# Optimization experiments

Hardware: AMD Instinct MI355X
Metric: run time of the kernel (lower is better)

The kernel has to match this reference:

```python
import jax, jax.numpy as jnp
import numpy as np

B, T, D = 1, 1024, 1024
H = 16; HKV = 16; HD = D // H; R = 2; K = 3; LOWR = 32
HR = HKV * R                      # heads after harmonic expansion
OUTW = HKV * HD * 2 * R           # w_proj output width
SCALE = HD ** -0.5


def setup_inputs() -> dict:
    key = jax.random.key(0)
    ks = jax.random.split(key, 10)
    def rn(k, shape, sc=1.0):
        return jax.random.normal(k, shape, dtype=jnp.float32) * sc
    return {
        'hidden_states': rn(ks[0], (B, T, D)),
        'q_w': rn(ks[1], (D, D), D ** -0.5),
        'k_w': rn(ks[2], (D, D), D ** -0.5),
        'v_w': rn(ks[3], (D, D), D ** -0.5),
        'w1': rn(ks[4], (LOWR, D), D ** -0.5),
        'w2': rn(ks[5], (OUTW, LOWR), LOWR ** -0.5),
        'conv_w': rn(ks[6], (OUTW, K), K ** -0.5),
        'bt_w': rn(ks[7], (HKV * R, D), D ** -0.5),
        'bt_b': jnp.zeros((HKV * R,), jnp.float32),
        'o_w': rn(ks[8], (D, D * R), (D * R) ** -0.5),
        'omega': 0.01 * jnp.ones((1, 1, 1, R), jnp.float32),
        'phi': jnp.zeros((1, 1, 1, R), jnp.float32),
    }


def path_attention_forward(hidden_states, q_w, k_w, v_w, w1, w2, conv_w,
                           bt_w, bt_b, o_w, omega, phi):
    b, t, _ = hidden_states.shape
    q = hidden_states @ q_w.T
    k = hidden_states @ k_w.T
    v = hidden_states @ v_w.T
    # low-rank w projection, causal depthwise short conv (kernel K), SiLU
    w_raw = (hidden_states @ w1.T) @ w2.T                    # [b,t,OUTW]
    xp = jnp.pad(w_raw, ((0, 0), (K - 1, 0), (0, 0)))
    w_raw = sum(xp[:, i:i + t, :] * conv_w[:, i] for i in range(K))
    w_raw = jax.nn.silu(w_raw)
    # rotary-like harmonic mixing of Householder directions
    w5 = w_raw.reshape(b, t, HKV, 2 * R, HD)
    Ah = w5[:, :, :, 0::2, :]                                # [b,t,HKV,R,HD]
    Bh = w5[:, :, :, 1::2, :]
    pos = jnp.arange(t, dtype=jnp.float32)[None, :, None, None]
    theta = omega * pos + phi                                # [1,t,1,R]
    c = jnp.cos(theta)[..., None]
    s = jnp.sin(theta)[..., None]
    Wdir = Ah * c + Bh * s
    Wdir = Wdir * jax.lax.rsqrt(jnp.sum(Wdir * Wdir, -1, keepdims=True) + 1e-6)
    beta = jax.nn.sigmoid(hidden_states @ bt_w.T + bt_b) * 2.0   # [b,t,HR]
    # repeat-interleave q/k/v heads across harmonics -> [b,HR,t,HD]
    to_h = lambda x: jnp.swapaxes(jnp.repeat(x.reshape(b, t, H, HD), R, axis=2), 1, 2)
    qh, kh, vh = to_h(q), to_h(k), to_h(v)
    wh = jnp.swapaxes(Wdir.reshape(b, t, HR, HD), 1, 2)      # [b,HR,t,HD]
    bh = jnp.swapaxes(beta, 1, 2)                            # [b,HR,t]
    # PaTH logits: A_ij = q_i^T (H_i ... H_{j+1}) k_j, H_t = I - beta_t w_t w_t^T.
    # WY/UT transform: with M_ts = beta_t (w_t.w_s) for s<t, the coefficients
    # B_tj (t>j) of the accumulated rank-1 corrections solve the unit-lower
    # triangular system (I + M) B = strilow(Db W K^T), and
    # A = tril(Q K^T - tril(Q W^T) B).
    idx = jnp.arange(t)
    strict = idx[:, None] > idx[None, :]
    incl = idx[:, None] >= idx[None, :]
    Mw = jnp.where(strict, jnp.einsum('bhtd,bhsd->bhts', wh, wh) * bh[..., None], 0.0)
    rhs = jnp.where(strict, jnp.einsum('bhtd,bhjd->bhtj', wh, kh) * bh[..., None], 0.0)
    Bmat = jax.scipy.linalg.solve_triangular(Mw + jnp.eye(t, dtype=Mw.dtype), rhs, lower=True)
    qk = jnp.einsum('bhid,bhjd->bhij', qh, kh)
    qw = jnp.where(incl, jnp.einsum('bhid,bhtd->bhit', qh, wh), 0.0)
    logits = (qk - jnp.einsum('bhit,bhtj->bhij', qw, Bmat)) * SCALE
    logits = jnp.where(incl, logits, -1e30)
    p = jax.nn.softmax(logits, axis=-1)
    o = jnp.einsum('bhij,bhjd->bhid', p, vh)                 # [b,HR,t,HD]
    o = jnp.swapaxes(o, 1, 2).reshape(b, t, HR * HD)         # [b,t,D*R]
    return o @ o_w.T


def reference(hidden_states, q_w, k_w, v_w, w1, w2, conv_w, bt_w, bt_b, o_w, omega, phi):
    return path_attention_forward(hidden_states, q_w, k_w, v_w, w1, w2, conv_w,
                                  bt_w, bt_b, o_w, omega, phi)
```

## Files before the change

kernel.cpp:

```cpp
#include <hip/hip_runtime.h>
#include <math.h>

#define TTD 1024
#define DDM 1024
#define HDIM 64
#define NOUTW 4096
#define PSCALE 0.125f
#define PSC2 0.18033688011112042f
#define LS 72

typedef __attribute__((ext_vector_type(8))) __bf16 bf16x8;
typedef __attribute__((ext_vector_type(4))) float f32x4;
#define MFMA16(a,b,c) __builtin_amdgcn_mfma_f32_16x16x32_bf16(a,b,c,0,0,0)

#define STR_(x) #x
#define WAITVM(N) asm volatile("s_waitcnt vmcnt(" STR_(N) ")" ::: "memory")
#define BAR() do { __builtin_amdgcn_s_barrier(); asm volatile("" ::: "memory"); } while (0)
#define LGKBAR() do { asm volatile("s_waitcnt lgkmcnt(0)" ::: "memory"); \
                      __builtin_amdgcn_s_barrier(); asm volatile("" ::: "memory"); } while (0)
#define FULLBAR() do { asm volatile("s_waitcnt vmcnt(0) lgkmcnt(0)" ::: "memory"); \
                       __builtin_amdgcn_s_barrier(); asm volatile("" ::: "memory"); } while (0)

__device__ __forceinline__ ushort f2b(float f) {
  unsigned u = __builtin_bit_cast(unsigned, f);
  return (ushort)((u + 0x7fffu + ((u >> 16) & 1u)) >> 16);
}
__device__ __forceinline__ float b2f(ushort u) {
  unsigned v = (unsigned)u << 16;
  return __builtin_bit_cast(float, v);
}

__device__ __forceinline__ void gload_lds16(const ushort* g, ushort* l) {
  __builtin_amdgcn_global_load_lds(
      (const __attribute__((address_space(1))) unsigned*)g,
      (__attribute__((address_space(3))) unsigned*)l, 16, 0, 0);
}

#define SWZ(row, cc) (((row) * 8 + ((cc) ^ ((row) & 7))) * 8)
#define SWZE(row, col) (SWZ(row, (col) >> 3) + ((col) & 7))

__device__ __forceinline__ void stage_tile(const ushort* gb, long gs, ushort* tile,
                                           int w, int l) {
  int sub = l >> 3, cc = (l & 7) ^ sub;
  #pragma unroll
  for (int it = 0; it < 2; ++it) {
    int q = w * 2 + it;
    gload_lds16(gb + (long)(q * 8 + sub) * gs + cc * 8, &tile[(q * 64 + l) * 8]);
  }
}

__device__ __forceinline__ bf16x8 frag(const ushort* tile, int row, int cc) {
  return *(const bf16x8*)&tile[SWZ(row, cc)];
}

#define OFF_X     0L
#define OFF_PZ    67108864L
#define OFF_HSB   67108864L
#define OFF_QWW   69206016L
#define OFF_KWW   71303168L
#define OFF_VWW   73400320L
#define OFF_W2B   75497472L
#define OFF_WLOWB 75759616L
#define OFF_TB    130023424L
#define OFF_OALL  130023424L
#define OFF_YB    134217728L
#define OFF_OWB   134217728L
#define OFF_WHB   138412032L
#define OFF_QB    142606336L
#define OFF_KB    144703488L
#define OFF_VTB   146800640L
#define OFF_BETA  148897792L
#define OFF_BW64  149159936L

__global__ __launch_bounds__(256) void cvt_kernel(const float* __restrict__ x,
                                                  ushort* __restrict__ y, long n) {
  long i = ((long)blockIdx.x * 256 + threadIdx.x) * 4;
  if (i >= n) return;
  float4 f = *(const float4*)(x + i);
  ushort4 o;
  o.x = f2b(f.x); o.y = f2b(f.y); o.z = f2b(f.z); o.w = f2b(f.w);
  *(ushort4*)(y + i) = o;
}

#define CVT_TOTAL 4390912L
struct CvtSegs {
  const float* src[7];
  ushort* dst[7];
  long cnt[7];
};
__global__ __launch_bounds__(256) void cvt_all_kernel(CvtSegs sg) {
  long e = ((long)blockIdx.x * 256 + threadIdx.x) * 4;
  #pragma unroll
  for (int s = 0; s < 7; ++s) {
    if (e < sg.cnt[s]) {
      float4 f = *(const float4*)(sg.src[s] + e);
      ushort4 o;
      o.x = f2b(f.x); o.y = f2b(f.y); o.z = f2b(f.z); o.w = f2b(f.w);
      *(ushort4*)(sg.dst[s] + e) = o;
      return;
    }
    e -= sg.cnt[s];
  }
}

__global__ __launch_bounds__(256) void qkv_sp_kernel(
    const ushort* __restrict__ hsb,
    const ushort* __restrict__ wq, const ushort* __restrict__ wk, const ushort* __restrict__ wv,
    const ushort* __restrict__ bw, const float* __restrict__ bt_b,
    ushort* __restrict__ cq, ushort* __restrict__ ck, ushort* __restrict__ cv,
    float* __restrict__ beta, ushort* __restrict__ wlowb)
{
  int z = blockIdx.z;
  if (z == 3 && blockIdx.x != 0) return;
  const ushort* B = (z == 0) ? wq : (z == 1) ? wk : (z == 2) ? wv : bw;

  __shared__ ushort Ab[2][8192];
  __shared__ ushort Bb[2][4096];

  int tid = threadIdx.x, w = tid >> 6, l = tid & 63;
  int quad = l >> 4, lane15 = l & 15;
  int rm = blockIdx.y * 128, cn = (z == 3) ? 0 : blockIdx.x * 64;
  const ushort* Ag = hsb + (long)rm * DDM;
  const ushort* Bg = B + (long)cn * DDM;

  stage_tile(Ag, DDM, &Ab[0][0], w, l);
  stage_tile(Ag + 64 * DDM, DDM, &Ab[0][4096], w, l);
  stage_tile(Bg, DDM, &Bb[0][0], w, l);

  f32x4 acc[2][4] = {};
  int arow0 = (w & 1) * 32 + lane15;
  int asel = (w >> 1) * 4096;
  for (int kt = 0; kt < 16; ++kt) {
    int cur = kt & 1;
    if (kt < 15) {
      int nxt = cur ^ 1;
      stage_tile(Ag + (kt + 1) * 64, DDM, &Ab[nxt][0], w, l);
      stage_tile(Ag + 64 * DDM + (kt + 1) * 64, DDM, &Ab[nxt][4096], w, l);
      stage_tile(Bg + (kt + 1) * 64, DDM, &Bb[nxt][0], w, l);
      WAITVM(6);
    } else {
      WAITVM(0);
    }
    BAR();
    const ushort* Atile = &Ab[cur][asel];
    #pragma unroll
    for (int s = 0; s < 2; ++s) {
      bf16x8 a0 = frag(Atile, arow0, s * 4 + quad);
      bf16x8 a1 = frag(Atile, arow0 + 16, s * 4 + quad);
      #pragma unroll
      for (int f = 0; f < 4; ++f) {
        bf16x8 bf = frag(&Bb[cur][0], f * 16 + lane15, s * 4 + quad);
        acc[0][f] = MFMA16(a0, bf, acc[0][f]);
        acc[1][f] = MFMA16(a1, bf, acc[1][f]);
      }
    }
    BAR();
  }

  if (z < 2) {
    ushort* Cb = (z == 0) ? cq : ck;
    #pragma unroll
    for (int rr = 0; rr < 2; ++rr) {
      int orow = rm + w * 32 + rr * 16 + quad * 4;
      #pragma unroll
      for (int f = 0; f < 4; ++f)
        #pragma unroll
        for (int r = 0; r < 4; ++r)
          Cb[(long)(orow + r) * DDM + cn + f * 16 + lane15] = f2b(acc[rr][f][r]);
    }
  } else if (z == 2) {
    #pragma unroll
    for (int rr = 0; rr < 2; ++rr) {
      int orow = rm + w * 32 + rr * 16 + quad * 4;
      #pragma unroll
      for (int f = 0; f < 4; ++f) {
        ushort4 o;
        o.x = f2b(acc[rr][f][0]); o.y = f2b(acc[rr][f][1]);
        o.z = f2b(acc[rr][f][2]); o.w = f2b(acc[rr][f][3]);
        *(ushort4*)&cv[(long)(cn + f * 16 + lane15) * TTD + orow] = o;
      }
    }
  } else {
    #pragma unroll
    for (int rr = 0; rr < 2; ++rr) {
      int orow = rm + w * 32 + rr * 16 + quad * 4;
      #pragma unroll
      for (int f = 0; f < 2; ++f) {
        int hr = f * 16 + lane15;
        float bb = bt_b[hr];
        #pragma unroll
        for (int r = 0; r < 4; ++r)
          beta[(long)hr * TTD + orow + r] = 2.f / (1.f + expf(-(acc[rr][f][r] + bb)));
      }
      #pragma unroll
      for (int f = 2; f < 4; ++f)
        #pragma unroll
        for (int r = 0; r < 4; ++r)
          wlowb[(long)(orow + r) * 32 + (f - 2) * 16 + lane15] = f2b(acc[rr][f][r]);
    }
  }
}

__global__ __launch_bounds__(256) void wrawconv_kernel(
    const ushort* __restrict__ wlowb, const ushort* __restrict__ w2b,
    const float* __restrict__ conv_w, const float* __restrict__ omega,
    const float* __restrict__ phi, ushort* __restrict__ whb)
{
  int rm = blockIdx.x * 64;
  int p = blockIdx.y;
  int hkv = p >> 1, r = p & 1;
  int c0 = hkv * 256 + r * 128;

  __shared__ ushort As[64 * 32];
  __shared__ ushort Bs[128 * 32];
  __shared__ float WR[66][132];

  int tid = threadIdx.x, w = tid >> 6, l = tid & 63;
  int quad = l >> 4, lane15 = l & 15;

  {
    int row = tid >> 2, ch = (tid & 3) * 8;
    gload_lds16(wlowb + (long)(rm + row) * 32 + ch, &As[row * 32 + ch]);
    gload_lds16(w2b + (long)(c0 + row) * 32 + ch, &Bs[row * 32 + ch]);
    gload_lds16(w2b + (long)(c0 + 64 + row) * 32 + ch, &Bs[(64 + row) * 32 + ch]);
  }
  {
    int hr2 = tid >> 7, col = tid & 127;
    float acc = 0.f;
    if (rm > 0) {
      long t = rm - 2 + hr2;
      for (int k = 0; k < 32; ++k)
        acc += b2f(wlowb[t * 32 + k]) * b2f(w2b[(long)(c0 + col) * 32 + k]);
    }
    WR[hr2][col] = acc;
  }
  FULLBAR();

  #pragma unroll
  for (int g = 0; g < 2; ++g) {
    f32x4 acc[4] = {};
    bf16x8 af = *(const bf16x8*)&As[(w * 16 + lane15) * 32 + quad * 8];
    #pragma unroll
    for (int f = 0; f < 4; ++f) {
      bf16x8 bf = *(const bf16x8*)&Bs[(g * 64 + f * 16 + lane15) * 32 + quad * 8];
      acc[f] = MFMA16(af, bf, acc[f]);
    }
    #pragma unroll
    for (int f = 0; f < 4; ++f)
      #pragma unroll
      for (int rr = 0; rr < 4; ++rr)
        WR[2 + w * 16 + quad * 4 + rr][g * 64 + f * 16 + lane15] = acc[f][rr];
  }
  LGKBAR();

  float cwa[3], cwb[3];
  #pragma unroll
  for (int i = 0; i < 3; ++i) {
    cwa[i] = conv_w[(long)(c0 + l) * 3 + i];
    cwb[i] = conv_w[(long)(c0 + 64 + l) * 3 + i];
  }
  float om = omega[r], ph = phi[r];
  for (int it = 0; it < 16; ++it) {
    int tl = it * 4 + w;
    int t = rm + tl;
    float a = cwa[0] * WR[tl][l] + cwa[1] * WR[tl + 1][l] + cwa[2] * WR[tl + 2][l];
    float b = cwb[0] * WR[tl][64 + l] + cwb[1] * WR[tl + 1][64 + l] + cwb[2] * WR[tl + 2][64 + l];
    a = a / (1.f + expf(-a));
    b = b / (1.f + expf(-b));
    float th = om * (float)t + ph;
    float wd = a * cosf(th) + b * sinf(th);
    float ss = wd * wd;
    #pragma unroll
    for (int o = 32; o > 0; o >>= 1) ss += __shfl_xor(ss, o, 64);
    whb[((long)p * TTD + t) * HDIM + l] = f2b(wd * (1.f / sqrtf(ss + 1e-6f)));
  }
}

__global__ __launch_bounds__(256) void solveA_kernel(
    const ushort* __restrict__ whb, const float* __restrict__ beta,
    ushort* __restrict__ TB, ushort* __restrict__ YB)
{
  int c = blockIdx.x, h = blockIdx.y;
  const ushort* whc = whb + ((long)h * TTD + c * 64) * HDIM;
  const float* bet = beta + (long)h * TTD + c * 64;
  ushort* TBh = TB + ((long)h * 16 + c) * 4096;
  ushort* YBh = YB + ((long)h * 16 + c) * 4096;

  __shared__ float Lm[64][65];
  __shared__ float Vf[64][65];
  __shared__ ushort WT[64 * LS];
  __shared__ ushort Tb[64 * LS];

  int tid = threadIdx.x, w = tid >> 6, l = tid & 63;
  int quad = l >> 4, lane15 = l & 15;

  f32x4 g[4] = {};
  #pragma unroll
  for (int s = 0; s < 2; ++s) {
    bf16x8 af = *(const bf16x8*)&whc[(long)(w * 16 + lane15) * HDIM + s * 32 + quad * 8];
    #pragma unroll
    for (int f = 0; f < 4; ++f) {
      bf16x8 bf = *(const bf16x8*)&whc[(long)(f * 16 + lane15) * HDIM + s * 32 + quad * 8];
      g[f] = MFMA16(af, bf, g[f]);
    }
  }
  #pragma unroll
  for (int r = 0; r < 4; ++r) {
    int t = w * 16 + quad * 4 + r;
    float bv = bet[t];
    #pragma unroll
    for (int f = 0; f < 4; ++f) {
      int tp = f * 16 + lane15;
      Lm[t][tp] = (t > tp) ? bv * g[f][r] : 0.f;
    }
  }
  {
    int d0 = (tid & 7) * 8;
    #pragma unroll
    for (int it = 0; it < 2; ++it) {
      int t = it * 32 + (tid >> 3);
      uint4 pk = *(const uint4*)&whc[(long)t * HDIM + d0];
      const ushort* pu = (const ushort*)&pk;
      #pragma unroll
      for (int i = 0; i < 8; ++i) WT[(d0 + i) * LS + t] = pu[i];
    }
  }
  LGKBAR();

  {
    float cur[16];
    #pragma unroll
    for (int i = 0; i < 16; ++i) cur[i] = (w * 16 + i == l) ? bet[l] : 0.f;
    for (int sb = 0; sb < 4; ++sb) {
      if (w == sb) {
        float xloc[16];
        #pragma unroll
        for (int i = 0; i < 16; ++i) {
          float bv = cur[i];
          #pragma unroll
          for (int j2 = 0; j2 < 16; ++j2)
            if (j2 < i) bv -= Lm[sb * 16 + i][sb * 16 + j2] * xloc[j2];
          xloc[i] = bv;
          Vf[sb * 16 + i][l] = bv;
        }
      }
      LGKBAR();
      if (w > sb) {
        float xp[16];
        #pragma unroll
        for (int t = 0; t < 16; ++t) xp[t] = Vf[sb * 16 + t][l];
        #pragma unroll
        for (int i = 0; i < 16; ++i) {
          float s2 = cur[i];
          #pragma unroll
          for (int t = 0; t < 16; ++t) s2 -= Lm[w * 16 + i][sb * 16 + t] * xp[t];
          cur[i] = s2;
        }
      }
    }
  }
  {
    int t = tid >> 2, off = (tid & 3) * 16;
    ushort tmp[16];
    #pragma unroll
    for (int i = 0; i < 16; ++i) { tmp[i] = f2b(Vf[t][off + i]); Tb[t * LS + off + i] = tmp[i]; }
    *(uint4*)&TBh[t * 64 + off] = *(const uint4*)&tmp[0];
    *(uint4*)&TBh[t * 64 + off + 8] = *(const uint4*)&tmp[8];
  }
  LGKBAR();
  f32x4 y[4] = {};
  #pragma unroll
  for (int s = 0; s < 2; ++s) {
    bf16x8 af = *(const bf16x8*)&Tb[(w * 16 + lane15) * LS + s * 32 + quad * 8];
    #pragma unroll
    for (int f = 0; f < 4; ++f) {
      bf16x8 bf = *(const bf16x8*)&WT[(f * 16 + lane15) * LS + s * 32 + quad * 8];
      y[f] = MFMA16(af, bf, y[f]);
    }
  }
  #pragma unroll
  for (int f = 0; f < 4; ++f)
    #pragma unroll
    for (int r = 0; r < 4; ++r)
      YBh[(long)(w * 16 + quad * 4 + r) * 64 + f * 16 + lane15] = f2b(y[f][r]);
}

__global__ __launch_bounds__(256) void solveB_kernel(
    const ushort* __restrict__ whb, const ushort* __restrict__ kb,
    const ushort* __restrict__ TB, const ushort* __restrict__ YB,
    ushort* __restrict__ Xb, ushort* __restrict__ KZ)
{
  int h = blockIdx.x;
  int ty = blockIdx.y;
  int js = (ty < 8) ? ty : (23 - ty);
  int j0 = js * 64;
  const ushort* wh_h = whb + (long)h * TTD * HDIM;
  const ushort* k_h = kb + (long)(h >> 1) * 64;
  ushort* X_h = Xb + (long)h * TTD * TTD;
  ushort* KZ_h = KZ + (long)h * 15 * TTD * HDIM;

  __shared__ ushort KT[4096];
  __shared__ ushort WT[4096];
  __shared__ ushort XM[4096];
  __shared__ ushort nS[4096];

  int tid = threadIdx.x, w = tid >> 6, l = tid & 63;
  int quad = l >> 4, lane15 = l & 15;
  f32x4 Sacc[4] = {}, Wacc[4] = {};

  stage_tile(k_h + (long)j0 * DDM, DDM, KT, w, l);

  float kreg[4][4];
  #pragma unroll
  for (int f = 0; f < 4; ++f)
    #pragma unroll
    for (int r = 0; r < 4; ++r)
      kreg[f][r] = b2f(k_h[(long)(j0 + w * 16 + quad * 4 + r) * DDM + f * 16 + lane15]);

  WAITVM(0);

  for (int c = js; c < 16; ++c) {
    const ushort* whc = wh_h + (long)c * 64 * HDIM;
    LGKBAR();
    {
      int d0 = (tid & 7) * 8;
      #pragma unroll
      for (int it = 0; it < 2; ++it) {
        int t = it * 32 + (tid >> 3);
        uint4 pk = *(const uint4*)&whc[(long)t * HDIM + d0];
        const ushort* pu = (const ushort*)&pk;
        #pragma unroll
        for (int i = 0; i < 8; ++i) WT[SWZE(d0 + i, t)] = pu[i];
      }
    }
    f32x4 xacc[4] = {};
    if (c == js) {
      f32x4 m[4] = {};
      #pragma unroll
      for (int s = 0; s < 2; ++s) {
        bf16x8 af = *(const bf16x8*)&whc[(long)(w * 16 + lane15) * HDIM + s * 32 + quad * 8];
        #pragma unroll
        for (int f = 0; f < 4; ++f)
          m[f] = MFMA16(af, frag(KT, f * 16 + lane15, s * 4 + quad), m[f]);
      }
      #pragma unroll
      for (int f = 0; f < 4; ++f)
        #pragma unroll
        for (int r = 0; r < 4; ++r) {
          int t = w * 16 + quad * 4 + r, j = f * 16 + lane15;
          XM[SWZE(j, t)] = (t > j) ? f2b(m[f][r]) : (ushort)0;
        }
      LGKBAR();
      const ushort* TBh = TB + ((long)h * 16 + c) * 4096;
      #pragma unroll
      for (int s = 0; s < 2; ++s) {
        bf16x8 af = *(const bf16x8*)&TBh[(long)(w * 16 + lane15) * 64 + s * 32 + quad * 8];
        #pragma unroll
        for (int f = 0; f < 4; ++f)
          xacc[f] = MFMA16(af, frag(XM, f * 16 + lane15, s * 4 + quad), xacc[f]);
      }
      LGKBAR();
    } else {
      const ushort* YBh = YB + ((long)h * 16 + c) * 4096;
      #pragma unroll
      for (int s = 0; s < 2; ++s) {
        bf16x8 af = *(const bf16x8*)&YBh[(long)(w * 16 + lane15) * 64 + s * 32 + quad * 8];
        #pragma unroll
        for (int f = 0; f < 4; ++f) {
          xacc[f] = MFMA16(af, frag(KT, f * 16 + lane15, s * 4 + quad), xacc[f]);
          xacc[f] = MFMA16(af, frag(nS, f * 16 + lane15, s * 4 + quad), xacc[f]);
        }
      }
    }
    #pragma unroll
    for (int f = 0; f < 4; ++f)
      #pragma unroll
      for (int r = 0; r < 4; ++r)
        XM[SWZE(f * 16 + lane15, w * 16 + quad * 4 + r)] = f2b(xacc[f][r]);
    LGKBAR();
    {
      int j = tid >> 2, c2 = (tid & 3) * 2;
      bf16x8 s0 = frag(XM, j, c2);
      bf16x8 s1 = frag(XM, j, c2 + 1);
      *(bf16x8*)&X_h[(long)(j0 + j) * TTD + c * 64 + c2 * 8] = s0;
      *(bf16x8*)&X_h[(long)(j0 + j) * TTD + c * 64 + c2 * 8 + 8] = s1;
    }
    if (c < 15) {
      #pragma unroll
      for (int s = 0; s < 2; ++s) {
        bf16x8 aw = frag(WT, w * 16 + lane15, s * 4 + quad);
        bf16x8 ax = frag(XM, w * 16 + lane15, s * 4 + quad);
        #pragma unroll
        for (int f = 0; f < 4; ++f) {
          Sacc[f] = MFMA16(aw, frag(XM, f * 16 + lane15, s * 4 + quad), Sacc[f]);
          Wacc[f] = MFMA16(ax, frag(WT, f * 16 + lane15, s * 4 + quad), Wacc[f]);
        }
      }
      ushort* pz = KZ_h + (long)c * TTD * HDIM;
      #pragma unroll
      for (int f = 0; f < 4; ++f)
        #pragma unroll
        for (int r = 0; r < 4; ++r)
          pz[(long)(j0 + w * 16 + quad * 4 + r) * 64 + f * 16 + lane15] =
              f2b(kreg[f][r] - Wacc[f][r]);
      #pragma unroll
      for (int f = 0; f < 4; ++f)
        #pragma unroll
        for (int r = 0; r < 4; ++r)
          nS[SWZE(f * 16 + lane15, w * 16 + quad * 4 + r)] = f2b(-Sacc[f][r]);
    }
  }
}

__global__ __launch_bounds__(256) void flash_kernel(
    const ushort* __restrict__ qb, const ushort* __restrict__ kbuf,
    const ushort* __restrict__ whb, const ushort* __restrict__ Xb,
    const ushort* __restrict__ KZ, const ushort* __restrict__ vTb,
    ushort* __restrict__ oall)
{
  int h = blockIdx.x;
  int y = blockIdx.y;
  int ri = (y < 8) ? y : (23 - y);
  int r0 = ri * 64;
  const ushort* q_h = qb + (long)(h >> 1) * 64;
  const ushort* k_h = kbuf + (long)(h >> 1) * 64;
  const ushort* wh_h = whb + (long)h * TTD * HDIM;
  const ushort* X_h = Xb + (long)h * TTD * TTD;
  const ushort* kz = KZ + ((long)h * 15 + (ri - 1)) * TTD * HDIM;
  const ushort* v_h = vTb + (long)(h >> 1) * 64 * TTD;

  __shared__ ushort S[2][3][4096];
  __shared__ ushort KD[4096];
  __shared__ ushort QWD[4096];
  __shared__ ushort PT[4096];

  int tid = threadIdx.x, w = tid >> 6, l = tid & 63;
  int quad = l >> 4, lane15 = l & 15;

  bf16x8 aq[2];
  #pragma unroll
  for (int s = 0; s < 2; ++s)
    aq[s] = *(const bf16x8*)&q_h[(long)(r0 + w * 16 + lane15) * DDM + s * 32 + quad * 8];
  stage_tile(k_h + (long)r0 * DDM, DDM, KD, w, l);
  if (ri > 0) stage_tile(kz, 64, &S[0][0][0], w, l);
  stage_tile(X_h + r0, TTD, &S[0][1][0], w, l);
  stage_tile(v_h, TTD, &S[0][2][0], w, l);
  {
    f32x4 t4[4] = {};
    #pragma unroll
    for (int s = 0; s < 2; ++s)
      #pragma unroll
      for (int f = 0; f < 4; ++f) {
        bf16x8 bf = *(const bf16x8*)&wh_h[(long)(r0 + f * 16 + lane15) * HDIM + s * 32 + quad * 8];
        t4[f] = MFMA16(aq[s], bf, t4[f]);
      }
    #pragma unroll
    for (int f = 0; f < 4; ++f)
      #pragma unroll
      for (int r = 0; r < 4; ++r) {
        int i = w * 16 + quad * 4 + r, t = f * 16 + lane15;
        QWD[SWZE(i, t)] = (i >= t) ? f2b(-t4[f][r]) : (ushort)0;
      }
  }

  f32x4 O[4] = {};
  float m[4], lsum[4];
  #pragma unroll
  for (int r = 0; r < 4; ++r) { m[r] = -1e30f; lsum[r] = 0.f; }

  for (int jb = 0; jb <= ri; ++jb) {
    int cur = jb & 1;
    if (jb < ri) {
      long c0n = (long)(jb + 1) * 64;
      ushort* nb = &S[cur ^ 1][0][0];
      if (jb + 1 < ri) {
        stage_tile(kz + c0n * 64, 64, nb, w, l);
        stage_tile(X_h + c0n * TTD + r0, TTD, nb + 4096, w, l);
        stage_tile(v_h + c0n, TTD, nb + 8192, w, l);
        WAITVM(6);
      } else {
        stage_tile(X_h + c0n * TTD + r0, TTD, nb + 4096, w, l);
        stage_tile(v_h + c0n, TTD, nb + 8192, w, l);
        WAITVM(4);
      }
    } else {
      WAITVM(0);
    }
    BAR();
    const ushort* Skz = &S[cur][0][0];
    const ushort* Sx  = &S[cur][1][0];
    const ushort* Sv  = &S[cur][2][0];
    f32x4 acc[4] = {};
    const ushort* Sb = (jb < ri) ? Skz : KD;
    #pragma unroll
    for (int s = 0; s < 2; ++s)
      #pragma unroll
      for (int f = 0; f < 4; ++f)
        acc[f] = MFMA16(aq[s], frag(Sb, f * 16 + lane15, s * 4 + quad), acc[f]);
    #pragma unroll
    for (int s = 0; s < 2; ++s) {
      bf16x8 aw = frag(QWD, w * 16 + lane15, s * 4 + quad);
      #pragma unroll
      for (int f = 0; f < 4; ++f)
        acc[f] = MFMA16(aw, frag(Sx, f * 16 + lane15, s * 4 + quad), acc[f]);
    }
    float rmax[4] = {-3e38f, -3e38f, -3e38f, -3e38f};
    #pragma unroll
    for (int f = 0; f < 4; ++f)
      #pragma unroll
      for (int r = 0; r < 4; ++r) {
        float lv = acc[f][r] * PSC2;
        if (jb == ri && (f * 16 + lane15) > (w * 16 + quad * 4 + r)) lv = -3e38f;
        acc[f][r] = lv;
        rmax[r] = fmaxf(rmax[r], lv);
      }
    #pragma unroll
    for (int r = 0; r < 4; ++r) {
      rmax[r] = fmaxf(rmax[r], __shfl_xor(rmax[r], 1, 64));
      rmax[r] = fmaxf(rmax[r], __shfl_xor(rmax[r], 2, 64));
      rmax[r] = fmaxf(rmax[r], __shfl_xor(rmax[r], 4, 64));
      rmax[r] = fmaxf(rmax[r], __shfl_xor(rmax[r], 8, 64));
    }
    float alpha[4], rs[4] = {0.f, 0.f, 0.f, 0.f};
    #pragma unroll
    for (int r = 0; r < 4; ++r) {
      float nm = fmaxf(m[r], rmax[r]);
      alpha[r] = exp2f(m[r] - nm);
      m[r] = nm;
    }
    #pragma unroll
    for (int f = 0; f < 4; ++f)
      #pragma unroll
      for (int r = 0; r < 4; ++r) {
        float e = exp2f(acc[f][r] - m[r]);
        acc[f][r] = e;
        rs[r] += e;
      }
    #pragma unroll
    for (int r = 0; r < 4; ++r) {
      rs[r] += __shfl_xor(rs[r], 1, 64);
      rs[r] += __shfl_xor(rs[r], 2, 64);
      rs[r] += __shfl_xor(rs[r], 4, 64);
      rs[r] += __shfl_xor(rs[r], 8, 64);
      lsum[r] = lsum[r] * alpha[r] + rs[r];
    }
    #pragma unroll
    for (int f = 0; f < 4; ++f)
      #pragma unroll
      for (int r = 0; r < 4; ++r) O[f][r] *= alpha[r];
    #pragma unroll
    for (int f = 0; f < 4; ++f)
      #pragma unroll
      for (int r = 0; r < 4; ++r) {
        int i = w * 16 + quad * 4 + r;
        PT[SWZE(i, f * 16 + lane15)] = f2b(acc[f][r]);
      }
    #pragma unroll
    for (int s = 0; s < 2; ++s) {
      bf16x8 ap = frag(PT, w * 16 + lane15, s * 4 + quad);
      #pragma unroll
      for (int f = 0; f < 4; ++f)
        O[f] = MFMA16(ap, frag(Sv, f * 16 + lane15, s * 4 + quad), O[f]);
    }
    BAR();
  }
  #pragma unroll
  for (int r = 0; r < 4; ++r) lsum[r] = 1.f / lsum[r];
  #pragma unroll
  for (int f = 0; f < 4; ++f)
    #pragma unroll
    for (int r = 0; r < 4; ++r)
      oall[(long)(r0 + w * 16 + quad * 4 + r) * 2048 + h * 64 + f * 16 + lane15] =
          f2b(O[f][r] * lsum[r]);
}

__global__ __launch_bounds__(256) void gemm_out_kernel(
    const ushort* __restrict__ A, const ushort* __restrict__ Bb, float* __restrict__ C)
{
  __shared__ ushort Ab[2][8192];
  __shared__ ushort Bt[2][8192];
  int tid = threadIdx.x, w = tid >> 6, l = tid & 63;
  int quad = l >> 4, lane15 = l & 15;
  int rm = blockIdx.y * 64, cn = blockIdx.x * 64;
  const ushort* Ag = A + (long)rm * 2048;
  const ushort* Bg = Bb + (long)cn * 2048;

  stage_tile(Ag, 2048, &Ab[0][0], w, l);
  stage_tile(Ag + 64, 2048, &Ab[0][4096], w, l);
  stage_tile(Bg, 2048, &Bt[0][0], w, l);
  stage_tile(Bg + 64, 2048, &Bt[0][4096], w, l);

  f32x4 acc[4] = {};
  for (int kt = 0; kt < 16; ++kt) {
    int cur = kt & 1;
    if (kt < 15) {
      int nxt = cur ^ 1;
      long o = (long)(kt + 1) * 128;
      stage_tile(Ag + o, 2048, &Ab[nxt][0], w, l);
      stage_tile(Ag + o + 64, 2048, &Ab[nxt][4096], w, l);
      stage_tile(Bg + o, 2048, &Bt[nxt][0], w, l);
      stage_tile(Bg + o + 64, 2048, &Bt[nxt][4096], w, l);
      WAITVM(8);
    } else {
      WAITVM(0);
    }
    BAR();
    #pragma unroll
    for (int u = 0; u < 2; ++u)
      #pragma unroll
      for (int s = 0; s < 2; ++s) {
        bf16x8 af = frag(&Ab[cur][u * 4096], w * 16 + lane15, s * 4 + quad);
        #pragma unroll
        for (int f = 0; f < 4; ++f)
          acc[f] = MFMA16(af, frag(&Bt[cur][u * 4096], f * 16 + lane15, s * 4 + quad), acc[f]);
      }
    BAR();
  }
  int orow = rm + w * 16 + quad * 4;
  #pragma unroll
  for (int f = 0; f < 4; ++f)
    #pragma unroll
    for (int r = 0; r < 4; ++r)
      C[(long)(orow + r) * DDM + cn + f * 16 + lane15] = acc[f][r];
}

extern "C" void kernel_launch(void* const* d_in, const int* in_sizes, int n_in,
                              void* d_out, int out_size, void* d_ws, size_t ws_size,
                              hipStream_t stream) {
  const float* hs     = (const float*)d_in[0];
  const float* q_w    = (const float*)d_in[1];
  const float* k_w    = (const float*)d_in[2];
  const float* v_w    = (const float*)d_in[3];
  const float* w1     = (const float*)d_in[4];
  const float* w2     = (const float*)d_in[5];
  const float* conv_w = (const float*)d_in[6];
  const float* bt_w   = (const float*)d_in[7];
  const float* bt_b   = (const float*)d_in[8];
  const float* o_w    = (const float*)d_in[9];
  const float* omega  = (const float*)d_in[10];
  const float* phi    = (const float*)d_in[11];
  float* out = (float*)d_out;
  char* ws = (char*)d_ws;

  ushort* Xb     = (ushort*)(ws + OFF_X);
  ushort* KZb    = (ushort*)(ws + OFF_PZ);
  ushort* hs_b   = (ushort*)(ws + OFF_HSB);
  ushort* qw_wb  = (ushort*)(ws + OFF_QWW);
  ushort* kw_wb  = (ushort*)(ws + OFF_KWW);
  ushort* vw_wb  = (ushort*)(ws + OFF_VWW);
  ushort* w2_b   = (ushort*)(ws + OFF_W2B);
  ushort* wlow_b = (ushort*)(ws + OFF_WLOWB);
  ushort* TB     = (ushort*)(ws + OFF_TB);
  ushort* o_all  = (ushort*)(ws + OFF_OALL);
  ushort* YB     = (ushort*)(ws + OFF_YB);
  ushort* ow_b   = (ushort*)(ws + OFF_OWB);
  ushort* wh_b   = (ushort*)(ws + OFF_WHB);
  ushort* q_b    = (ushort*)(ws + OFF_QB);
  ushort* k_b    = (ushort*)(ws + OFF_KB);
  ushort* vT_b   = (ushort*)(ws + OFF_VTB);
  float*  beta   = (float*)(ws + OFF_BETA);
  ushort* bw_b   = (ushort*)(ws + OFF_BW64);

  CvtSegs sg;
  sg.src[0] = hs;   sg.dst[0] = hs_b;          sg.cnt[0] = 1048576;
  sg.src[1] = q_w;  sg.dst[1] = qw_wb;         sg.cnt[1] = 1048576;
  sg.src[2] = k_w;  sg.dst[2] = kw_wb;         sg.cnt[2] = 1048576;
  sg.src[3] = v_w;  sg.dst[3] = vw_wb;         sg.cnt[3] = 1048576;
  sg.src[4] = w2;   sg.dst[4] = w2_b;          sg.cnt[4] = 131072;
  sg.src[5] = bt_w; sg.dst[5] = bw_b;          sg.cnt[5] = 32768;
  sg.src[6] = w1;   sg.dst[6] = bw_b + 32768;  sg.cnt[6] = 32768;
  cvt_all_kernel<<<dim3((CVT_TOTAL + 1023) / 1024), 256, 0, stream>>>(sg);

  qkv_sp_kernel<<<dim3(16, 8, 4), 256, 0, stream>>>(
      hs_b, qw_wb, kw_wb, vw_wb, bw_b, bt_b, q_b, k_b, vT_b, beta, wlow_b);

  wrawconv_kernel<<<dim3(16, 32), 256, 0, stream>>>(
      wlow_b, w2_b, conv_w, omega, phi, wh_b);

  solveA_kernel<<<dim3(16, 32), 256, 0, stream>>>(wh_b, beta, TB, YB);
  solveB_kernel<<<dim3(32, 16), 256, 0, stream>>>(wh_b, k_b, TB, YB, Xb, KZb);

  cvt_kernel<<<dim3(2048), 256, 0, stream>>>(o_w, ow_b, 2097152L);

  flash_kernel<<<dim3(32, 16), 256, 0, stream>>>(q_b, k_b, wh_b, Xb, KZb, vT_b, o_all);

  gemm_out_kernel<<<dim3(16, 16), 256, 0, stream>>>(o_all, ow_b, out);

  (void)in_sizes; (void)n_in; (void)out_size; (void)ws_size;
}
```

Baseline: 231.6 us.

## Fuse w-direction conv into solveA, pack X triangularly, merge o_w conversion

Merges the w-projection/conv/SiLU/normalise kernel with the chunk-local triangular solve, so the normalised directions stay in shared memory instead of being read back from global memory. It also stores the X matrix as packed lower-triangular 64x64 tiles per head rather than a dense T x T matrix, which shrinks the workspace and makes the flash kernel's tile loads contiguous. The separate o_w conversion launch is folded into the batched conversion kernel. In exchange, shared memory is reused through a hand-laid-out pool with aliased regions, which may lower occupancy and is fragile.

```diff
diff --git a/kernel.cpp b/kernel.cpp
--- a/kernel.cpp
+++ b/kernel.cpp
@@ -4,7 +4,6 @@
 #define TTD 1024
 #define DDM 1024
 #define HDIM 64
-#define NOUTW 4096
 #define PSCALE 0.125f
 #define PSC2 0.18033688011112042f
 #define LS 72
@@ -53,45 +52,36 @@
   return *(const bf16x8*)&tile[SWZ(row, cc)];
 }
 
+#define XT_PERH   557056L
 #define OFF_X     0L
-#define OFF_PZ    67108864L
-#define OFF_HSB   67108864L
-#define OFF_QWW   69206016L
-#define OFF_KWW   71303168L
-#define OFF_VWW   73400320L
-#define OFF_W2B   75497472L
-#define OFF_WLOWB 75759616L
-#define OFF_TB    130023424L
-#define OFF_OALL  130023424L
-#define OFF_YB    134217728L
-#define OFF_OWB   134217728L
-#define OFF_WHB   138412032L
-#define OFF_QB    142606336L
-#define OFF_KB    144703488L
-#define OFF_VTB   146800640L
-#define OFF_BETA  148897792L
-#define OFF_BW64  149159936L
-
-__global__ __launch_bounds__(256) void cvt_kernel(const float* __restrict__ x,
-                                                  ushort* __restrict__ y, long n) {
-  long i = ((long)blockIdx.x * 256 + threadIdx.x) * 4;
-  if (i >= n) return;
-  float4 f = *(const float4*)(x + i);
-  ushort4 o;
-  o.x = f2b(f.x); o.y = f2b(f.y); o.z = f2b(f.z); o.w = f2b(f.w);
-  *(ushort4*)(y + i) = o;
-}
-
-#define CVT_TOTAL 4390912L
+#define OFF_PZ    35651584L
+#define OFF_HSB   35651584L
+#define OFF_QWW   37748736L
+#define OFF_KWW   39845888L
+#define OFF_VWW   41943040L
+#define OFF_W2B   44040192L
+#define OFF_WLOWB 44302336L
+#define OFF_TB    98566144L
+#define OFF_OALL  98566144L
+#define OFF_YB    102760448L
+#define OFF_OWB   106954752L
+#define OFF_WHB   111149056L
+#define OFF_QB    115343360L
+#define OFF_KB    117440512L
+#define OFF_VTB   119537664L
+#define OFF_BETA  121634816L
+#define OFF_BW64  121765888L
+
+#define CVT_TOTAL 6488064L
 struct CvtSegs {
-  const float* src[7];
-  ushort* dst[7];
-  long cnt[7];
+  const float* src[8];
+  ushort* dst[8];
+  long cnt[8];
 };
 __global__ __launch_bounds__(256) void cvt_all_kernel(CvtSegs sg) {
   long e = ((long)blockIdx.x * 256 + threadIdx.x) * 4;
   #pragma unroll
-  for (int s = 0; s < 7; ++s) {
+  for (int s = 0; s < 8; ++s) {
     if (e < sg.cnt[s]) {
       float4 f = *(const float4*)(sg.src[s] + e);
       ushort4 o;
@@ -201,19 +191,27 @@
   }
 }
 
-__global__ __launch_bounds__(256) void wrawconv_kernel(
+__global__ __launch_bounds__(256) void wraw_solveA_kernel(
     const ushort* __restrict__ wlowb, const ushort* __restrict__ w2b,
     const float* __restrict__ conv_w, const float* __restrict__ omega,
-    const float* __restrict__ phi, ushort* __restrict__ whb)
+    const float* __restrict__ phi, const float* __restrict__ beta,
+    ushort* __restrict__ whb, ushort* __restrict__ TB, ushort* __restrict__ YB)
 {
-  int rm = blockIdx.x * 64;
+  int c = blockIdx.x;
+  int rm = c * 64;
   int p = blockIdx.y;
   int hkv = p >> 1, r = p & 1;
   int c0 = hkv * 256 + r * 128;
 
-  __shared__ ushort As[64 * 32];
-  __shared__ ushort Bs[128 * 32];
-  __shared__ float WR[66][132];
+  __shared__ char pool_[65568];
+  ushort* As = (ushort*)pool_;
+  ushort* Bs = (ushort*)(pool_ + 4096);
+  float (*WR)[132] = (float(*)[132])(pool_ + 12288);
+  ushort* Wrow = (ushort*)(pool_ + 47136);
+  ushort* WT   = (ushort*)(pool_ + 56352);
+  float (*Lm)[65] = (float(*)[65])pool_;
+  float (*Vf)[65] = (float(*)[65])(pool_ + 16640);
+  ushort* Tb = (ushort*)(pool_ + 33280);
 
   int tid = threadIdx.x, w = tid >> 6, l = tid & 63;
   int quad = l >> 4, lane15 = l & 15;
@@ -253,76 +251,56 @@
   }
   LGKBAR();
 
-  float cwa[3], cwb[3];
-  #pragma unroll
-  for (int i = 0; i < 3; ++i) {
-    cwa[i] = conv_w[(long)(c0 + l) * 3 + i];
-    cwb[i] = conv_w[(long)(c0 + 64 + l) * 3 + i];
-  }
-  float om = omega[r], ph = phi[r];
-  for (int it = 0; it < 16; ++it) {
-    int tl = it * 4 + w;
-    int t = rm + tl;
-    float a = cwa[0] * WR[tl][l] + cwa[1] * WR[tl + 1][l] + cwa[2] * WR[tl + 2][l];
-    float b = cwb[0] * WR[tl][64 + l] + cwb[1] * WR[tl + 1][64 + l] + cwb[2] * WR[tl + 2][64 + l];
-    a = a / (1.f + expf(-a));
-    b = b / (1.f + expf(-b));
-    float th = om * (float)t + ph;
-    float wd = a * cosf(th) + b * sinf(th);
-    float ss = wd * wd;
-    #pragma unroll
-    for (int o = 32; o > 0; o >>= 1) ss += __shfl_xor(ss, o, 64);
-    whb[((long)p * TTD + t) * HDIM + l] = f2b(wd * (1.f / sqrtf(ss + 1e-6f)));
-  }
-}
-
-__global__ __launch_bounds__(256) void solveA_kernel(
-    const ushort* __restrict__ whb, const float* __restrict__ beta,
-    ushort* __restrict__ TB, ushort* __restrict__ YB)
-{
-  int c = blockIdx.x, h = blockIdx.y;
-  const ushort* whc = whb + ((long)h * TTD + c * 64) * HDIM;
-  const float* bet = beta + (long)h * TTD + c * 64;
-  ushort* TBh = TB + ((long)h * 16 + c) * 4096;
-  ushort* YBh = YB + ((long)h * 16 + c) * 4096;
-
-  __shared__ float Lm[64][65];
-  __shared__ float Vf[64][65];
-  __shared__ ushort WT[64 * LS];
-  __shared__ ushort Tb[64 * LS];
-
-  int tid = threadIdx.x, w = tid >> 6, l = tid & 63;
-  int quad = l >> 4, lane15 = l & 15;
-
-  f32x4 g[4] = {};
+  {
+    float cwa[3], cwb[3];
+    #pragma unroll
+    for (int i = 0; i < 3; ++i) {
+      cwa[i] = conv_w[(long)(c0 + l) * 3 + i];
+      cwb[i] = conv_w[(long)(c0 + 64 + l) * 3 + i];
+    }
+    float om = omega[r], ph = phi[r];
+    for (int it = 0; it < 16; ++it) {
+      int tl = it * 4 + w;
+      int t = rm + tl;
+      float a = cwa[0] * WR[tl][l] + cwa[1] * WR[tl + 1][l] + cwa[2] * WR[tl + 2][l];
+      float b = cwb[0] * WR[tl][64 + l] + cwb[1] * WR[tl + 1][64 + l] + cwb[2] * WR[tl + 2][64 + l];
+      a = a / (1.f + expf(-a));
+      b = b / (1.f + expf(-b));
+      float th = om * (float)t + ph;
+      float wd = a * cosf(th) + b * sinf(th);
+      float ss = wd * wd;
+      #pragma unroll
+      for (int o = 32; o > 0; o >>= 1) ss += __shfl_xor(ss, o, 64);
+      ushort hv = f2b(wd * (1.f / sqrtf(ss + 1e-6f)));
+      whb[((long)p * TTD + t) * HDIM + l] = hv;
+      Wrow[tl * LS + l] = hv;
+      WT[l * LS + tl] = hv;
+    }
+  }
+  LGKBAR();
+
+  const float* bet = beta + (long)p * TTD + rm;
+  ushort* TBh = TB + ((long)p * 16 + c) * 4096;
+  ushort* YBh = YB + ((long)p * 16 + c) * 4096;
+
+  f32x4 g4[4] = {};
   #pragma unroll
   for (int s = 0; s < 2; ++s) {
-    bf16x8 af = *(const bf16x8*)&whc[(long)(w * 16 + lane15) * HDIM + s * 32 + quad * 8];
+    bf16x8 af = *(const bf16x8*)&Wrow[(w * 16 + lane15) * LS + s * 32 + quad * 8];
     #pragma unroll
     for (int f = 0; f < 4; ++f) {
-      bf16x8 bf = *(const bf16x8*)&whc[(long)(f * 16 + lane15) * HDIM + s * 32 + quad * 8];
-      g[f] = MFMA16(af, bf, g[f]);
-    }
-  }
-  #pragma unroll
-  for (int r = 0; r < 4; ++r) {
-    int t = w * 16 + quad * 4 + r;
+      bf16x8 bf = *(const bf16x8*)&Wrow[(f * 16 + lane15) * LS + s * 32 + quad * 8];
+      g4[f] = MFMA16(af, bf, g4[f]);
+    }
+  }
+  #pragma unroll
+  for (int r4 = 0; r4 < 4; ++r4) {
+    int t = w * 16 + quad * 4 + r4;
     float bv = bet[t];
     #pragma unroll
     for (int f = 0; f < 4; ++f) {
       int tp = f * 16 + lane15;
-      Lm[t][tp] = (t > tp) ? bv * g[f][r] : 0.f;
-    }
-  }
-  {
-    int d0 = (tid & 7) * 8;
-    #pragma unroll
-    for (int it = 0; it < 2; ++it) {
-      int t = it * 32 + (tid >> 3);
-      uint4 pk = *(const uint4*)&whc[(long)t * HDIM + d0];
-      const ushort* pu = (const ushort*)&pk;
-      #pragma unroll
-      for (int i = 0; i < 8; ++i) WT[(d0 + i) * LS + t] = pu[i];
+      Lm[t][tp] = (t > tp) ? bv * g4[f][r4] : 0.f;
     }
   }
   LGKBAR();
@@ -381,8 +359,8 @@
   #pragma unroll
   for (int f = 0; f < 4; ++f)
     #pragma unroll
-    for (int r = 0; r < 4; ++r)
-      YBh[(long)(w * 16 + quad * 4 + r) * 64 + f * 16 + lane15] = f2b(y[f][r]);
+    for (int r4 = 0; r4 < 4; ++r4)
+      YBh[(long)(w * 16 + quad * 4 + r4) * 64 + f * 16 + lane15] = f2b(y[f][r4]);
 }
 
 __global__ __launch_bounds__(256) void solveB_kernel(
@@ -396,8 +374,9 @@
   int j0 = js * 64;
   const ushort* wh_h = whb + (long)h * TTD * HDIM;
   const ushort* k_h = kb + (long)(h >> 1) * 64;
-  ushort* X_h = Xb + (long)h * TTD * TTD;
+  ushort* X_h = Xb + (long)h * XT_PERH;
   ushort* KZ_h = KZ + (long)h * 15 * TTD * HDIM;
+  int xidx = js * 16 - js * (js - 1) / 2;
 
   __shared__ ushort KT[4096];
   __shared__ ushort WT[4096];
@@ -479,12 +458,14 @@
         XM[SWZE(f * 16 + lane15, w * 16 + quad * 4 + r)] = f2b(xacc[f][r]);
     LGKBAR();
     {
+      ushort* xt = X_h + (long)xidx * 4096;
       int j = tid >> 2, c2 = (tid & 3) * 2;
       bf16x8 s0 = frag(XM, j, c2);
       bf16x8 s1 = frag(XM, j, c2 + 1);
-      *(bf16x8*)&X_h[(long)(j0 + j) * TTD + c * 64 + c2 * 8] = s0;
-      *(bf16x8*)&X_h[(long)(j0 + j) * TTD + c * 64 + c2 * 8 + 8] = s1;
-    }
+      *(bf16x8*)&xt[j * 64 + c2 * 8] = s0;
+      *(bf16x8*)&xt[j * 64 + c2 * 8 + 8] = s1;
+    }
+    ++xidx;
     if (c < 15) {
       #pragma unroll
       for (int s = 0; s < 2; ++s) {
@@ -525,7 +506,7 @@
   const ushort* q_h = qb + (long)(h >> 1) * 64;
   const ushort* k_h = kbuf + (long)(h >> 1) * 64;
   const ushort* wh_h = whb + (long)h * TTD * HDIM;
-  const ushort* X_h = Xb + (long)h * TTD * TTD;
+  const ushort* X_h = Xb + (long)h * XT_PERH;
   const ushort* kz = KZ + ((long)h * 15 + (ri - 1)) * TTD * HDIM;
   const ushort* v_h = vTb + (long)(h >> 1) * 64 * TTD;
 
@@ -541,9 +522,10 @@
   #pragma unroll
   for (int s = 0; s < 2; ++s)
     aq[s] = *(const bf16x8*)&q_h[(long)(r0 + w * 16 + lane15) * DDM + s * 32 + quad * 8];
+  const ushort* xst = X_h + (long)ri * 4096;
   stage_tile(k_h + (long)r0 * DDM, DDM, KD, w, l);
   if (ri > 0) stage_tile(kz, 64, &S[0][0][0], w, l);
-  stage_tile(X_h + r0, TTD, &S[0][1][0], w, l);
+  stage_tile(xst, 64, &S[0][1][0], w, l);
   stage_tile(v_h, TTD, &S[0][2][0], w, l);
   {
     f32x4 t4[4] = {};
@@ -570,16 +552,17 @@
 
   for (int jb = 0; jb <= ri; ++jb) {
     int cur = jb & 1;
+    const ushort* xnx = xst + (long)(15 - jb) * 4096;
     if (jb < ri) {
       long c0n = (long)(jb + 1) * 64;
       ushort* nb = &S[cur ^ 1][0][0];
       if (jb + 1 < ri) {
         stage_tile(kz + c0n * 64, 64, nb, w, l);
-        stage_tile(X_h + c0n * TTD + r0, TTD, nb + 4096, w, l);
+        stage_tile(xnx, 64, nb + 4096, w, l);
         stage_tile(v_h + c0n, TTD, nb + 8192, w, l);
         WAITVM(6);
       } else {
-        stage_tile(X_h + c0n * TTD + r0, TTD, nb + 4096, w, l);
+        stage_tile(xnx, 64, nb + 4096, w, l);
         stage_tile(v_h + c0n, TTD, nb + 8192, w, l);
         WAITVM(4);
       }
@@ -663,6 +646,7 @@
         O[f] = MFMA16(ap, frag(Sv, f * 16 + lane15, s * 4 + quad), O[f]);
     }
     BAR();
+    xst = xnx;
   }
   #pragma unroll
   for (int r = 0; r < 4; ++r) lsum[r] = 1.f / lsum[r];
@@ -769,19 +753,17 @@
   sg.src[4] = w2;   sg.dst[4] = w2_b;          sg.cnt[4] = 131072;
   sg.src[5] = bt_w; sg.dst[5] = bw_b;          sg.cnt[5] = 32768;
   sg.src[6] = w1;   sg.dst[6] = bw_b + 32768;  sg.cnt[6] = 32768;
+  sg.src[7] = o_w;  sg.dst[7] = ow_b;          sg.cnt[7] = 2097152;
   cvt_all_kernel<<<dim3((CVT_TOTAL + 1023) / 1024), 256, 0, stream>>>(sg);
 
   qkv_sp_kernel<<<dim3(16, 8, 4), 256, 0, stream>>>(
       hs_b, qw_wb, kw_wb, vw_wb, bw_b, bt_b, q_b, k_b, vT_b, beta, wlow_b);
 
-  wrawconv_kernel<<<dim3(16, 32), 256, 0, stream>>>(
-      wlow_b, w2_b, conv_w, omega, phi, wh_b);
-
-  solveA_kernel<<<dim3(16, 32), 256, 0, stream>>>(wh_b, beta, TB, YB);
+  wraw_solveA_kernel<<<dim3(16, 32), 256, 0, stream>>>(
+      wlow_b, w2_b, conv_w, omega, phi, beta, wh_b, TB, YB);
+
   solveB_kernel<<<dim3(32, 16), 256, 0, stream>>>(wh_b, k_b, TB, YB, Xb, KZb);
 
-  cvt_kernel<<<dim3(2048), 256, 0, stream>>>(o_w, ow_b, 2097152L);
-
   flash_kernel<<<dim3(32, 16), 256, 0, stream>>>(q_b, k_b, wh_b, Xb, KZb, vT_b, o_all);
 
   gemm_out_kernel<<<dim3(16, 16), 256, 0, stream>>>(o_all, ow_b, out);
```

Result: faster. 224.0 us (-3.3%).
